# Optimization experiments

Hardware: AMD Instinct MI355X
Metric: run time of the kernel (lower is better)

Reference implementation:

```python
import jax, jax.numpy as jnp
import numpy as np

B, T, C, HS = 8, 2048, 1024, 64

def setup_inputs() -> dict:
    key = jax.random.key(0)
    ks = jax.random.split(key, 6)
    return {
        "q_vec": jax.random.normal(ks[0], (B, T, C), dtype=jnp.float32),
        "k_vec": jax.random.normal(ks[1], (B, T, C), dtype=jnp.float32),
        "v_vec": jax.random.normal(ks[2], (B, T, C), dtype=jnp.float32),
        "mask": jnp.ones((B, T), dtype=jnp.int32),
        "Wq": jax.random.normal(ks[3], (C, HS), dtype=jnp.float32) * (C ** -0.5),
        "Wk": jax.random.normal(ks[4], (C, HS), dtype=jnp.float32) * (C ** -0.5),
        "Wv": jax.random.normal(ks[5], (C, HS), dtype=jnp.float32) * (C ** -0.5),
    }

def reference(q_vec, k_vec, v_vec, mask, Wq, Wk, Wv):
    # bias-free linear projections: [B,T,C] @ [C,HS] -> [B,T,HS]
    q = jnp.einsum('btc,ch->bth', q_vec, Wq)
    k = jnp.einsum('btc,ch->bth', k_vec, Wk)
    v = jnp.einsum('btc,ch->bth', v_vec, Wv)
    scale = k.shape[-1] ** -0.5
    # full T x T score matrix, as in the original module
    scores = jnp.einsum('bth,bsh->bts', q, k) * scale  # [B,T,T]
    Tq = scores.shape[1]
    # _expand_along_time: expanded[b,i,j] = mask[b,j], then causal tril
    mask_exp = jnp.broadcast_to(mask[:, None, :].astype(jnp.float32), scores.shape)
    tril = jnp.tril(jnp.ones((Tq, Tq), dtype=jnp.float32))
    combined = mask_exp * tril[None, :, :]
    scores = jnp.where(combined == 0, -jnp.inf, scores)
    attn = jax.nn.softmax(scores, axis=-1)
    # dropout p=0.0 (eval) -> identity
    out = jnp.einsum('bts,bsh->bth', attn, v)  # [B,T,HS]
    return out
```

## Files before the change

### kernel.cpp

```cpp
#include <hip/hip_runtime.h>
#include <hip/hip_bf16.h>
#include <cmath>
#include <stdint.h>

#define B_ 8
#define T_ 2048
#define C_ 1024
#define HS_ 64
#define NS 8
#define LP 72
#define PKC 128
#define XLP2 136

typedef __attribute__((ext_vector_type(8))) short short8;
typedef __attribute__((ext_vector_type(4))) float floatx4;

__device__ inline unsigned short f2bf(float f) {
    union { float f; unsigned u; } v; v.f = f;
    unsigned r = v.u + 0x7FFF + ((v.u >> 16) & 1);
    return (unsigned short)(r >> 16);
}
__device__ inline unsigned pk2bf(float a, float b) {
    union { __hip_bfloat162 h; unsigned u; } v;
    v.h = __float22bfloat162_rn(float2{a, b});
    return v.u;
}
__device__ inline float bf2f(unsigned short u) {
    union { unsigned u; float f; } w; w.u = ((unsigned)u) << 16; return w.f;
}

__global__ __launch_bounds__(256) void prep_wt(const float* __restrict__ Wq,
                                               const float* __restrict__ Wk,
                                               const float* __restrict__ Wv,
                                               unsigned short* __restrict__ wt) {
    int p = blockIdx.x >> 4;
    int chunk = blockIdx.x & 15;
    const float* W = (p == 0) ? Wq : (p == 1) ? Wk : Wv;
    unsigned short* WT = wt + p * (C_ * HS_);
    int base = chunk * 4096;
    for (int i = threadIdx.x; i < 4096; i += 256) {
        int idx = base + i;
        int k = idx >> 6, n = idx & 63;
        WT[n * C_ + k] = f2bf(W[idx]);
    }
}

__global__ __launch_bounds__(256, 4) void proj_kernel(
    const float* __restrict__ qv, const float* __restrict__ kv, const float* __restrict__ vv,
    const unsigned short* __restrict__ wt,
    unsigned short* __restrict__ qb, unsigned short* __restrict__ kb, unsigned short* __restrict__ vb)
{
    __shared__ unsigned short Xl[64 * XLP2];
    __shared__ unsigned short Wl[64 * XLP2];

    const int bid  = blockIdx.x;
    const int p    = bid >> 8;
    const int tile = bid & 255;
    const float* X = (p == 0) ? qv : (p == 1) ? kv : vv;
    const unsigned short* WT = wt + p * (C_ * HS_);
    unsigned short* Ob = (p == 0) ? qb : (p == 1) ? kb : vb;
    const float oscale = (p == 0) ? 0.125f : 1.0f;

    const int tid = threadIdx.x;
    const int wave = tid >> 6, lane = tid & 63, quad = lane >> 4, l16 = lane & 15;
    const long rowbase = (long)tile * 64;
    const float* Xbase = X + rowbase * C_;

    const int xsub = lane & 31;
    const int xrp  = lane >> 5;
    const int wsub = lane & 15;
    const int wr4  = lane >> 4;

    floatx4 xf[8];
    short8  wf[4];

    #pragma unroll
    for (int i = 0; i < 8; ++i)
        xf[i] = *(const floatx4*)(Xbase + (wave * 16 + i * 2 + xrp) * C_ + xsub * 4);
    #pragma unroll
    for (int i = 0; i < 4; ++i)
        wf[i] = *(const short8*)(WT + (wave * 16 + i * 4 + wr4) * C_ + wsub * 8);

    floatx4 acc[4] = { {0,0,0,0},{0,0,0,0},{0,0,0,0},{0,0,0,0} };

    for (int c = 0; c < C_ / PKC; ++c) {
        #pragma unroll
        for (int i = 0; i < 8; ++i) {
            int row = wave * 16 + i * 2 + xrp;
            unsigned u0 = pk2bf(xf[i][0], xf[i][1]);
            unsigned u1 = pk2bf(xf[i][2], xf[i][3]);
            unsigned* d = (unsigned*)&Xl[row * XLP2 + xsub * 4];
            d[0] = u0; d[1] = u1;
        }
        #pragma unroll
        for (int i = 0; i < 4; ++i)
            *(short8*)&Wl[(wave * 16 + i * 4 + wr4) * XLP2 + wsub * 8] = wf[i];
        __syncthreads();

        if (c + 1 < C_ / PKC) {
            const int kc = (c + 1) * PKC;
            #pragma unroll
            for (int i = 0; i < 8; ++i)
                xf[i] = *(const floatx4*)(Xbase + (wave * 16 + i * 2 + xrp) * C_ + kc + xsub * 4);
            #pragma unroll
            for (int i = 0; i < 4; ++i)
                wf[i] = *(const short8*)(WT + (wave * 16 + i * 4 + wr4) * C_ + kc + wsub * 8);
        }

        #pragma unroll
        for (int kcc = 0; kcc < 4; ++kcc) {
            short8 af = *(short8*)&Xl[(wave * 16 + l16) * XLP2 + kcc * 32 + quad * 8];
            #pragma unroll
            for (int nt = 0; nt < 4; ++nt) {
                short8 bf = *(short8*)&Wl[(nt * 16 + l16) * XLP2 + kcc * 32 + quad * 8];
                acc[nt] = __builtin_amdgcn_mfma_f32_16x16x32_bf16(af, bf, acc[nt], 0, 0, 0);
            }
        }
        __syncthreads();
    }

    #pragma unroll
    for (int nt = 0; nt < 4; ++nt)
        #pragma unroll
        for (int r = 0; r < 4; ++r) {
            long row = rowbase + wave * 16 + quad * 4 + r;
            Ob[row * HS_ + nt * 16 + l16] = f2bf(acc[nt][r] * oscale);
        }
}

__global__ __launch_bounds__(256) void attn_partial(
    const unsigned short* __restrict__ qb, const unsigned short* __restrict__ kb,
    const unsigned short* __restrict__ vb, const int* __restrict__ mask,
    unsigned short* __restrict__ Opart, float* __restrict__ Mpart, float* __restrict__ Lpart)
{
    const int s  = blockIdx.x & (NS - 1);
    const int bq = blockIdx.x >> 3;
    const int qt = bq & 31;
    const int b  = bq >> 5;
    if (s > qt) return;

    __shared__ unsigned short Klds[64 * LP];
    __shared__ unsigned short Vt[64 * LP];
    __shared__ unsigned short Plds[4][16 * LP];

    const int tid = threadIdx.x;
    const int wave = tid >> 6, lane = tid & 63, quad = lane >> 4, l16 = lane & 15;

    const int qrow = qt * 64 + wave * 16 + l16;
    const unsigned short* qp = qb + ((long)(b * T_ + qrow)) * HS_;
    short8 aq0 = *(const short8*)&qp[0  + quad * 8];
    short8 aq1 = *(const short8*)&qp[32 + quad * 8];

    floatx4 acc_o[4] = { {0,0,0,0},{0,0,0,0},{0,0,0,0},{0,0,0,0} };
    float m_r[4] = { -INFINITY, -INFINITY, -INFINITY, -INFINITY };
    float l_r[4] = { 0.f, 0.f, 0.f, 0.f };

    const int rowg = qt * 64 + wave * 16 + quad * 4;

    const int skey = tid >> 3;
    const int sf8  = (tid & 7) * 8;
    const int vp = tid & 31, vg = tid >> 5;

    for (int c = s; c <= qt; c += NS) {
        const int kc = c * 64;
        #pragma unroll
        for (int it = 0; it < 2; ++it) {
            int key = it * 32 + skey;
            *(short8*)&Klds[key * LP + sf8] =
                *(const short8*)&kb[((long)(b * T_ + kc + key)) * HS_ + sf8];
        }
        {
            const unsigned short* v0p = &vb[((long)(b * T_ + kc + 2 * vp)) * HS_ + vg * 8];
            short8 v0 = *(const short8*)v0p;
            short8 v1 = *(const short8*)(v0p + HS_);
            #pragma unroll
            for (int j = 0; j < 8; ++j) {
                unsigned pr = (unsigned)(unsigned short)v0[j] |
                              ((unsigned)(unsigned short)v1[j] << 16);
                *(unsigned*)&Vt[(vg * 8 + j) * LP + 2 * vp] = pr;
            }
        }
        __syncthreads();

        floatx4 sv[4];
        #pragma unroll
        for (int kt = 0; kt < 4; ++kt) {
            floatx4 a = {0.f, 0.f, 0.f, 0.f};
            short8 bk0 = *(short8*)&Klds[(kt * 16 + l16) * LP + 0  + quad * 8];
            short8 bk1 = *(short8*)&Klds[(kt * 16 + l16) * LP + 32 + quad * 8];
            a = __builtin_amdgcn_mfma_f32_16x16x32_bf16(aq0, bk0, a, 0, 0, 0);
            a = __builtin_amdgcn_mfma_f32_16x16x32_bf16(aq1, bk1, a, 0, 0, 0);
            sv[kt] = a;
        }

        const bool lastc = (c == qt);
        #pragma unroll
        for (int kt = 0; kt < 4; ++kt) {
            int key = kc + kt * 16 + l16;
            int mk = mask[b * T_ + key];
            #pragma unroll
            for (int r = 0; r < 4; ++r) {
                bool dead = (mk == 0) || (lastc && key > rowg + r);
                if (dead) sv[kt][r] = -INFINITY;
            }
        }

        float alpha[4];
        #pragma unroll
        for (int r = 0; r < 4; ++r) {
            float mx = fmaxf(fmaxf(sv[0][r], sv[1][r]), fmaxf(sv[2][r], sv[3][r]));
            #pragma unroll
            for (int off = 1; off < 16; off <<= 1)
                mx = fmaxf(mx, __shfl_xor(mx, off));
            float mn = fmaxf(m_r[r], mx);
            float a_ = __expf(m_r[r] - mn);
            float ps = 0.f;
            #pragma unroll
            for (int kt = 0; kt < 4; ++kt) {
                float pv = __expf(sv[kt][r] - mn);
                sv[kt][r] = pv;
                ps += pv;
            }
            #pragma unroll
            for (int off = 1; off < 16; off <<= 1)
                ps += __shfl_xor(ps, off);
            l_r[r] = l_r[r] * a_ + ps;
            m_r[r] = mn;
            alpha[r] = a_;
        }
        #pragma unroll
        for (int nt = 0; nt < 4; ++nt)
            #pragma unroll
            for (int r = 0; r < 4; ++r)
                acc_o[nt][r] *= alpha[r];

        unsigned short* pl = Plds[wave];
        #pragma unroll
        for (int kt = 0; kt < 4; ++kt)
            #pragma unroll
            for (int r = 0; r < 4; ++r)
                pl[(quad * 4 + r) * LP + kt * 16 + l16] = f2bf(sv[kt][r]);
        short8 ap0 = *(short8*)&pl[l16 * LP + 0  + quad * 8];
        short8 ap1 = *(short8*)&pl[l16 * LP + 32 + quad * 8];

        #pragma unroll
        for (int nt = 0; nt < 4; ++nt) {
            short8 bv0 = *(short8*)&Vt[(nt * 16 + l16) * LP + 0  + quad * 8];
            short8 bv1 = *(short8*)&Vt[(nt * 16 + l16) * LP + 32 + quad * 8];
            acc_o[nt] = __builtin_amdgcn_mfma_f32_16x16x32_bf16(ap0, bv0, acc_o[nt], 0, 0, 0);
            acc_o[nt] = __builtin_amdgcn_mfma_f32_16x16x32_bf16(ap1, bv1, acc_o[nt], 0, 0, 0);
        }
        __syncthreads();
    }

    unsigned short* Op = Opart + (long)blockIdx.x * 4096;
    #pragma unroll
    for (int nt = 0; nt < 4; ++nt)
        #pragma unroll
        for (int r = 0; r < 4; ++r)
            Op[(wave * 16 + quad * 4 + r) * 64 + nt * 16 + l16] = f2bf(acc_o[nt][r]);
    if (l16 == 0) {
        #pragma unroll
        for (int r = 0; r < 4; ++r) {
            int rl = wave * 16 + quad * 4 + r;
            Mpart[(long)blockIdx.x * 64 + rl] = m_r[r];
            Lpart[(long)blockIdx.x * 64 + rl] = l_r[r];
        }
    }
}

__global__ __launch_bounds__(256) void attn_combine(
    const unsigned short* __restrict__ Opart, const float* __restrict__ Mpart,
    const float* __restrict__ Lpart, float* __restrict__ out)
{
    const int half = blockIdx.x & 1;
    const int bq = blockIdx.x >> 1;
    const int qt = bq & 31;
    const int b  = bq >> 5;
    const int nsp = (qt + 1 < NS) ? qt + 1 : NS;

    const int row  = (threadIdx.x >> 3) + half * 32;
    const int colg = (threadIdx.x & 7) * 8;
    const long base = (long)bq * NS;

    float M = -INFINITY;
    #pragma unroll
    for (int sp = 0; sp < NS; ++sp)
        if (sp < nsp) M = fmaxf(M, Mpart[(base + sp) * 64 + row]);

    float w[NS];
    float L = 0.f;
    #pragma unroll
    for (int sp = 0; sp < NS; ++sp)
        if (sp < nsp) {
            float e = __expf(Mpart[(base + sp) * 64 + row] - M);
            w[sp] = e;
            L += e * Lpart[(base + sp) * 64 + row];
        }

    float acc[8] = {0,0,0,0,0,0,0,0};
    #pragma unroll
    for (int sp = 0; sp < NS; ++sp)
        if (sp < nsp) {
            const unsigned short* Op = Opart + (base + sp) * 4096 + row * 64 + colg;
            short8 o = *(const short8*)Op;
            float ws = w[sp];
            #pragma unroll
            for (int j = 0; j < 8; ++j)
                acc[j] += ws * bf2f((unsigned short)o[j]);
        }

    float inv = 1.0f / L;
    float* op = out + ((long)(b * T_ + qt * 64 + row)) * HS_ + colg;
    floatx4 o0 = { acc[0] * inv, acc[1] * inv, acc[2] * inv, acc[3] * inv };
    floatx4 o1 = { acc[4] * inv, acc[5] * inv, acc[6] * inv, acc[7] * inv };
    *(floatx4*)op = o0;
    *(floatx4*)(op + 4) = o1;
}

extern "C" void kernel_launch(void* const* d_in, const int* in_sizes, int n_in,
                              void* d_out, int out_size, void* d_ws, size_t ws_size,
                              hipStream_t stream)
{
    const float* qv = (const float*)d_in[0];
    const float* kv = (const float*)d_in[1];
    const float* vv = (const float*)d_in[2];
    const int*   mask = (const int*)d_in[3];
    const float* Wq = (const float*)d_in[4];
    const float* Wk = (const float*)d_in[5];
    const float* Wv = (const float*)d_in[6];
    float* out = (float*)d_out;

    unsigned short* wt    = (unsigned short*)d_ws;
    unsigned short* qbuf  = wt + 3 * C_ * HS_;
    unsigned short* kbuf  = qbuf + (long)B_ * T_ * HS_;
    unsigned short* vbuf  = kbuf + (long)B_ * T_ * HS_;
    unsigned short* Opart = vbuf + (long)B_ * T_ * HS_;
    float* Mpart = (float*)(Opart + (long)B_ * 32 * NS * 4096);
    float* Lpart = Mpart + (long)B_ * 32 * NS * 64;

    prep_wt<<<48, 256, 0, stream>>>(Wq, Wk, Wv, wt);
    proj_kernel<<<768, 256, 0, stream>>>(qv, kv, vv, wt, qbuf, kbuf, vbuf);
    attn_partial<<<B_ * 32 * NS, 256, 0, stream>>>(qbuf, kbuf, vbuf, mask, Opart, Mpart, Lpart);
    attn_combine<<<B_ * 32 * 2, 256, 0, stream>>>(Opart, Mpart, Lpart, out);
}
```

Before: 260.7 us.

## Load projection MFMA operands directly from global memory, drop LDS staging

The projection kernel no longer stages X and W tiles through shared memory with block-wide barriers. Each wave now owns an independent 16-row tile and loads its MFMA operands straight from global memory into registers, with one-step register prefetch. The fp32-to-bf16 conversion happens in registers. This removes LDS traffic and __syncthreads, but each lane's global loads are narrower and less coalesced, and the weight fragments are now reloaded per wave rather than shared across a block.

```diff
diff --git a/kernel.cpp b/kernel.cpp
--- a/kernel.cpp
+++ b/kernel.cpp
@@ -9,8 +9,6 @@
 #define HS_ 64
 #define NS 8
 #define LP 72
-#define PKC 128
-#define XLP2 136
 
 typedef __attribute__((ext_vector_type(8))) short short8;
 typedef __attribute__((ext_vector_type(4))) float floatx4;
@@ -45,87 +43,66 @@
     }
 }
 
-__global__ __launch_bounds__(256, 4) void proj_kernel(
+__global__ __launch_bounds__(256) void proj_kernel(
     const float* __restrict__ qv, const float* __restrict__ kv, const float* __restrict__ vv,
     const unsigned short* __restrict__ wt,
     unsigned short* __restrict__ qb, unsigned short* __restrict__ kb, unsigned short* __restrict__ vb)
 {
-    __shared__ unsigned short Xl[64 * XLP2];
-    __shared__ unsigned short Wl[64 * XLP2];
-
-    const int bid  = blockIdx.x;
-    const int p    = bid >> 8;
-    const int tile = bid & 255;
+    const int tid  = threadIdx.x;
+    const int wave = tid >> 6, lane = tid & 63, quad = lane >> 4, l16 = lane & 15;
+    const int wid  = blockIdx.x * 4 + wave;
+    const int p    = wid >> 10;
+    const int tile = wid & 1023;
+
     const float* X = (p == 0) ? qv : (p == 1) ? kv : vv;
     const unsigned short* WT = wt + p * (C_ * HS_);
     unsigned short* Ob = (p == 0) ? qb : (p == 1) ? kb : vb;
     const float oscale = (p == 0) ? 0.125f : 1.0f;
 
-    const int tid = threadIdx.x;
-    const int wave = tid >> 6, lane = tid & 63, quad = lane >> 4, l16 = lane & 15;
-    const long rowbase = (long)tile * 64;
-    const float* Xbase = X + rowbase * C_;
-
-    const int xsub = lane & 31;
-    const int xrp  = lane >> 5;
-    const int wsub = lane & 15;
-    const int wr4  = lane >> 4;
-
-    floatx4 xf[8];
-    short8  wf[4];
-
-    #pragma unroll
-    for (int i = 0; i < 8; ++i)
-        xf[i] = *(const floatx4*)(Xbase + (wave * 16 + i * 2 + xrp) * C_ + xsub * 4);
-    #pragma unroll
-    for (int i = 0; i < 4; ++i)
-        wf[i] = *(const short8*)(WT + (wave * 16 + i * 4 + wr4) * C_ + wsub * 8);
+    const float* xp = X + ((long)tile * 16 + l16) * C_ + quad * 8;
+    const unsigned short* wp = WT + l16 * C_ + quad * 8;
 
     floatx4 acc[4] = { {0,0,0,0},{0,0,0,0},{0,0,0,0},{0,0,0,0} };
 
-    for (int c = 0; c < C_ / PKC; ++c) {
-        #pragma unroll
-        for (int i = 0; i < 8; ++i) {
-            int row = wave * 16 + i * 2 + xrp;
-            unsigned u0 = pk2bf(xf[i][0], xf[i][1]);
-            unsigned u1 = pk2bf(xf[i][2], xf[i][3]);
-            unsigned* d = (unsigned*)&Xl[row * XLP2 + xsub * 4];
-            d[0] = u0; d[1] = u1;
-        }
-        #pragma unroll
-        for (int i = 0; i < 4; ++i)
-            *(short8*)&Wl[(wave * 16 + i * 4 + wr4) * XLP2 + wsub * 8] = wf[i];
-        __syncthreads();
-
-        if (c + 1 < C_ / PKC) {
-            const int kc = (c + 1) * PKC;
-            #pragma unroll
-            for (int i = 0; i < 8; ++i)
-                xf[i] = *(const floatx4*)(Xbase + (wave * 16 + i * 2 + xrp) * C_ + kc + xsub * 4);
-            #pragma unroll
-            for (int i = 0; i < 4; ++i)
-                wf[i] = *(const short8*)(WT + (wave * 16 + i * 4 + wr4) * C_ + kc + wsub * 8);
-        }
-
-        #pragma unroll
-        for (int kcc = 0; kcc < 4; ++kcc) {
-            short8 af = *(short8*)&Xl[(wave * 16 + l16) * XLP2 + kcc * 32 + quad * 8];
-            #pragma unroll
-            for (int nt = 0; nt < 4; ++nt) {
-                short8 bf = *(short8*)&Wl[(nt * 16 + l16) * XLP2 + kcc * 32 + quad * 8];
-                acc[nt] = __builtin_amdgcn_mfma_f32_16x16x32_bf16(af, bf, acc[nt], 0, 0, 0);
-            }
-        }
-        __syncthreads();
+    floatx4 xa, xb;
+    short8 bfr0, bfr1, bfr2, bfr3;
+    xa = *(const floatx4*)(xp);
+    xb = *(const floatx4*)(xp + 4);
+    bfr0 = *(const short8*)(wp + 0 * 16 * C_);
+    bfr1 = *(const short8*)(wp + 1 * 16 * C_);
+    bfr2 = *(const short8*)(wp + 2 * 16 * C_);
+    bfr3 = *(const short8*)(wp + 3 * 16 * C_);
+
+    #pragma unroll 4
+    for (int ks = 0; ks < 32; ++ks) {
+        floatx4 cx0 = xa, cx1 = xb;
+        short8 cb0 = bfr0, cb1 = bfr1, cb2 = bfr2, cb3 = bfr3;
+        if (ks + 1 < 32) {
+            const int k0 = (ks + 1) * 32;
+            xa = *(const floatx4*)(xp + k0);
+            xb = *(const floatx4*)(xp + k0 + 4);
+            bfr0 = *(const short8*)(wp + 0 * 16 * C_ + k0);
+            bfr1 = *(const short8*)(wp + 1 * 16 * C_ + k0);
+            bfr2 = *(const short8*)(wp + 2 * 16 * C_ + k0);
+            bfr3 = *(const short8*)(wp + 3 * 16 * C_ + k0);
+        }
+        union { short8 s; unsigned u[4]; } af;
+        af.u[0] = pk2bf(cx0[0], cx0[1]);
+        af.u[1] = pk2bf(cx0[2], cx0[3]);
+        af.u[2] = pk2bf(cx1[0], cx1[1]);
+        af.u[3] = pk2bf(cx1[2], cx1[3]);
+        acc[0] = __builtin_amdgcn_mfma_f32_16x16x32_bf16(af.s, cb0, acc[0], 0, 0, 0);
+        acc[1] = __builtin_amdgcn_mfma_f32_16x16x32_bf16(af.s, cb1, acc[1], 0, 0, 0);
+        acc[2] = __builtin_amdgcn_mfma_f32_16x16x32_bf16(af.s, cb2, acc[2], 0, 0, 0);
+        acc[3] = __builtin_amdgcn_mfma_f32_16x16x32_bf16(af.s, cb3, acc[3], 0, 0, 0);
     }
 
+    unsigned short* op = Ob + ((long)tile * 16 + quad * 4) * HS_ + l16;
     #pragma unroll
     for (int nt = 0; nt < 4; ++nt)
         #pragma unroll
-        for (int r = 0; r < 4; ++r) {
-            long row = rowbase + wave * 16 + quad * 4 + r;
-            Ob[row * HS_ + nt * 16 + l16] = f2bf(acc[nt][r] * oscale);
-        }
+        for (int r = 0; r < 4; ++r)
+            op[r * HS_ + nt * 16] = f2bf(acc[nt][r] * oscale);
 }
 
 __global__ __launch_bounds__(256) void attn_partial(
```

Measured after the change: 276.3 us. 6.0% more time.
